# Optimization experiments

Measured on AMD Instinct MI355X. Metric: run time of the kernel, lower is better.

The kernel has to match this reference:

```python
import jax, jax.numpy as jnp
import numpy as np

EMBED_DIM = 768
NUM_HEADS = 12
HEAD_DIM = EMBED_DIM // NUM_HEADS
WINDOW = 64
B, S = 2, 2048


def setup_inputs() -> dict:
    key = jax.random.key(0)
    ks = jax.random.split(key, 8)
    xavier = 0.1 * np.sqrt(6.0 / (EMBED_DIM + EMBED_DIM))  # xavier_uniform with gain=0.1
    def lin_w(k):
        return jax.random.uniform(k, (EMBED_DIM, EMBED_DIM), jnp.float32, -xavier, xavier)
    return {
        "query": jax.random.normal(ks[0], (B, S, EMBED_DIM), jnp.float32),
        "key": jax.random.normal(ks[1], (B, S, EMBED_DIM), jnp.float32),
        "value": jax.random.normal(ks[2], (B, S, EMBED_DIM), jnp.float32),
        "key_padding_mask": jnp.zeros((B, S), dtype=bool),
        "Wq": lin_w(ks[3]), "bq": jnp.zeros((EMBED_DIM,), jnp.float32),
        "Wk": lin_w(ks[4]), "bk": jnp.zeros((EMBED_DIM,), jnp.float32),
        "Wv": lin_w(ks[5]), "bv": jnp.zeros((EMBED_DIM,), jnp.float32),
        "Wo": lin_w(ks[6]), "bo": jnp.zeros((EMBED_DIM,), jnp.float32),
    }


def reference(query, key, value, key_padding_mask, Wq, bq, Wk, bk, Wv, bv, Wo, bo):
    Bsz, Sl, E = query.shape
    H, D = NUM_HEADS, HEAD_DIM

    def proj(x, W, b):  # nn.Linear: x @ W.T + b, then split heads -> [B,H,S,D]
        return (x @ W.T + b).reshape(Bsz, Sl, H, D).transpose(0, 2, 1, 3)

    q = proj(query, Wq, bq)
    k = proj(key, Wk, bk)
    v = proj(value, Wv, bv)

    scale = float(D) ** -0.5
    scores = jnp.einsum("bhqd,bhkd->bhqk", q, k) * scale  # [B,H,S,S]

    idx = jnp.arange(Sl)
    win_mask = jnp.abs(idx[:, None] - idx[None, :]) > WINDOW  # True = masked out
    scores = jnp.where(win_mask[None, None], -10000.0, scores)
    scores = jnp.where(key_padding_mask[:, None, None, :], -10000.0, scores)
    scores = jnp.where(jnp.isnan(scores), -10000.0, scores)

    attn = jax.nn.softmax(scores, axis=-1) + 1e-6
    attn = jnp.where(jnp.isnan(attn), 1.0 / Sl, attn)

    ctx = jnp.einsum("bhqk,bhkd->bhqd", attn, v)
    ctx = ctx.transpose(0, 2, 1, 3).reshape(Bsz, Sl, E)
    out = ctx @ Wo.T + bo
    out = jnp.where(jnp.isnan(out), value, out)
    return out, attn
```

## Files before the change

### kernel.cpp

```cpp
#include <hip/hip_runtime.h>
#include <hip/hip_bf16.h>

#define EMBED 768
#define NHEADS 12
#define HDIM 64
#define WIN 64
#define BATCH 2
#define SEQ 2048
#define MROWS (BATCH*SEQ)
#define NBH (BATCH*NHEADS)
#define QT 32
#define KP 160
#define KPAD 168
#define SPAD 164

typedef __attribute__((ext_vector_type(8))) short short8;
typedef __attribute__((ext_vector_type(4))) float f32x4;

__device__ __forceinline__ float bf2f(unsigned short u) {
    union { unsigned int i; float f; } z;
    z.i = ((unsigned int)u) << 16;
    return z.f;
}
__device__ __forceinline__ unsigned short f2bf(float f) {
    __hip_bfloat16 h = __float2bfloat16(f);
    return *reinterpret_cast<unsigned short*>(&h);
}

__device__ __forceinline__ void gload16(const unsigned short* g, unsigned short* l) {
    __builtin_amdgcn_global_load_lds(
        (const __attribute__((address_space(1))) unsigned int*)g,
        (__attribute__((address_space(3))) unsigned int*)l,
        16, 0, 0);
}

struct CvtArgs {
    const float* src[4];
    unsigned short* dst[4];
};

__global__ __launch_bounds__(256) void cvt_w(CvtArgs ca) {
    const int n4 = EMBED * EMBED / 4;
    const int bper = (n4 + 255) / 256;
    int seg = blockIdx.x / bper;
    int i = (blockIdx.x - seg * bper) * 256 + threadIdx.x;
    if (i < n4) {
        float4 v = reinterpret_cast<const float4*>(ca.src[seg])[i];
        ushort4 o;
        o.x = f2bf(v.x); o.y = f2bf(v.y); o.z = f2bf(v.z); o.w = f2bf(v.w);
        reinterpret_cast<ushort4*>(ca.dst[seg])[i] = o;
    }
}

struct GArgs {
    const void* A[3];
    const unsigned short* Bm[3];
    const float* bias[3];
    void* C[3];
};

template<int F32OUT, int F32A>
__global__ __launch_bounds__(256) void gemm_nt(GArgs ga, int M, int N, int K) {
    const int z = blockIdx.z;
    const unsigned short* __restrict__ Bm = ga.Bm[z];
    const float* __restrict__ bias = ga.bias[z];

    const int bm = blockIdx.y * 128;
    const int bn = blockIdx.x * 128;

    __shared__ unsigned short As[128 * 32];
    __shared__ unsigned short Bs[128 * 32];

    const int tid = threadIdx.x;
    const int lane = tid & 63;
    const int wid = tid >> 6;
    const int wm = wid >> 1, wn = wid & 1;

    f32x4 acc[4][4] = {};

    const int fr = lane & 15;
    const int krow = (lane >> 4) * 8;

    for (int k0 = 0; k0 < K; k0 += 32) {
#pragma unroll
        for (int it = 0; it < 2; ++it) {
            int idx = it * 256 + tid;
            int r = idx >> 2;
            int c = (idx & 3) * 8;
            if (F32A) {
                const float* Af = (const float*)ga.A[z];
                const float4* src = reinterpret_cast<const float4*>(
                    Af + (size_t)(bm + r) * K + k0 + c);
                float4 v0 = src[0], v1 = src[1];
                short8 o;
                unsigned short* ou = reinterpret_cast<unsigned short*>(&o);
                ou[0] = f2bf(v0.x); ou[1] = f2bf(v0.y);
                ou[2] = f2bf(v0.z); ou[3] = f2bf(v0.w);
                ou[4] = f2bf(v1.x); ou[5] = f2bf(v1.y);
                ou[6] = f2bf(v1.z); ou[7] = f2bf(v1.w);
                *reinterpret_cast<short8*>(&As[idx * 8]) = o;
            } else {
                const unsigned short* Ab = (const unsigned short*)ga.A[z];
                gload16(Ab + (size_t)(bm + r) * K + k0 + c, &As[idx * 8]);
            }
            gload16(Bm + (size_t)(bn + r) * K + k0 + c, &Bs[idx * 8]);
        }
        __syncthreads();

        short8 af[4], bfv[4];
#pragma unroll
        for (int mf = 0; mf < 4; ++mf)
            af[mf] = *reinterpret_cast<const short8*>(&As[(wm * 64 + mf * 16 + fr) * 32 + krow]);
#pragma unroll
        for (int nf = 0; nf < 4; ++nf)
            bfv[nf] = *reinterpret_cast<const short8*>(&Bs[(wn * 64 + nf * 16 + fr) * 32 + krow]);
#pragma unroll
        for (int mf = 0; mf < 4; ++mf)
#pragma unroll
            for (int nf = 0; nf < 4; ++nf)
                acc[mf][nf] = __builtin_amdgcn_mfma_f32_16x16x32_bf16(
                    af[mf], bfv[nf], acc[mf][nf], 0, 0, 0);
        __syncthreads();
    }

    const int fq = lane >> 4;
#pragma unroll
    for (int mf = 0; mf < 4; ++mf)
#pragma unroll
        for (int nf = 0; nf < 4; ++nf) {
            int col = bn + wn * 64 + nf * 16 + fr;
            float bv = bias[col];
#pragma unroll
            for (int r = 0; r < 4; ++r) {
                int row = bm + wm * 64 + mf * 16 + fq * 4 + r;
                float v = acc[mf][nf][r] + bv;
                if (F32OUT)
                    reinterpret_cast<float*>(ga.C[z])[(size_t)row * N + col] = v;
                else
                    reinterpret_cast<unsigned short*>(ga.C[z])[(size_t)row * N + col] = f2bf(v);
            }
        }
}

__global__ __launch_bounds__(256) void sumv_kernel(const unsigned short* __restrict__ Vb,
                                                   float* __restrict__ sumV) {
    __shared__ float r[32][HDIM];
    const int bh = blockIdx.x;
    const int b = bh / NHEADS, h = bh % NHEADS;
    const int dg = (threadIdx.x & 7) * 8;
    const int r0 = threadIdx.x >> 3;
    float acc[8] = {};
    const unsigned short* vp = Vb + (size_t)(b * SEQ) * EMBED + h * HDIM + dg;
    for (int j = r0; j < SEQ; j += 32) {
        short8 v = *reinterpret_cast<const short8*>(vp + (size_t)j * EMBED);
#pragma unroll
        for (int e = 0; e < 8; ++e)
            acc[e] += bf2f(((const unsigned short*)&v)[e]);
    }
#pragma unroll
    for (int e = 0; e < 8; ++e) r[r0][dg + e] = acc[e];
    __syncthreads();
    if (threadIdx.x < HDIM) {
        float s = 0.f;
#pragma unroll
        for (int i = 0; i < 32; ++i) s += r[i][threadIdx.x];
        sumV[bh * HDIM + threadIdx.x] = s;
    }
}

__global__ __launch_bounds__(256, 3) void attn_mfma(
    const unsigned short* __restrict__ Q,
    const unsigned short* __restrict__ Kb,
    const unsigned short* __restrict__ Vb,
    const unsigned char* __restrict__ kpm,
    const float* __restrict__ sumV,
    float* __restrict__ attn_out,
    unsigned short* __restrict__ ctx) {
    const int qt = blockIdx.x;
    const int bh = blockIdx.y;
    const int h = bh % NHEADS;
    const int b = bh / NHEADS;
    const int q0 = qt * QT;
    const int kstart = max(q0 - WIN, 0);

    __shared__ float Sf[QT][SPAD];
    __shared__ unsigned short Pb[QT][KPAD];
    __shared__ unsigned short Vt[HDIM][KPAD];

    const int tid = threadIdx.x;
    const int l = tid & 63;
    const int w = tid >> 6;
    const int fr = l & 15;
    const int ksl = (l >> 4) * 8;

    const size_t base = (size_t)(b * SEQ) * EMBED + h * HDIM;

    {
        const int mf = w >> 1;
        const int nt0 = (w & 1) * 5;

        const unsigned short* qrow = Q + base + (size_t)(q0 + mf * 16 + fr) * EMBED;
        short8 aq0 = *reinterpret_cast<const short8*>(qrow + ksl);
        short8 aq1 = *reinterpret_cast<const short8*>(qrow + 32 + ksl);

        f32x4 sacc[5] = {};
#pragma unroll
        for (int t = 0; t < 5; ++t) {
            int jg = kstart + (nt0 + t) * 16 + fr;
            int jc = min(jg, SEQ - 1);
            const unsigned short* krow = Kb + base + (size_t)jc * EMBED;
            short8 b0 = *reinterpret_cast<const short8*>(krow + ksl);
            short8 b1 = *reinterpret_cast<const short8*>(krow + 32 + ksl);
            sacc[t] = __builtin_amdgcn_mfma_f32_16x16x32_bf16(aq0, b0, sacc[t], 0, 0, 0);
            sacc[t] = __builtin_amdgcn_mfma_f32_16x16x32_bf16(aq1, b1, sacc[t], 0, 0, 0);
        }

#pragma unroll
        for (int t = 0; t < 5; ++t) {
            int col = (nt0 + t) * 16 + fr;
            int jg = kstart + col;
            bool jvalid = (jg < SEQ);
            bool mk = jvalid && kpm[b * SEQ + jg];
#pragma unroll
            for (int r = 0; r < 4; ++r) {
                int rowl = mf * 16 + (l >> 4) * 4 + r;
                int qi = q0 + rowl;
                float s = sacc[t][r] * 0.125f;
                if (mk) s = -10000.f;
                int dd = qi - jg;
                if (!jvalid || dd > WIN || dd < -WIN) s = -1e30f;
                Sf[rowl][col] = s;
            }
        }

#pragma unroll
        for (int pass = 0; pass < 5; ++pass) {
            int jrel = pass * 32 + (tid >> 3);
            int jg = kstart + jrel;
            int dg = (tid & 7) * 8;
            short8 v = {};
            if (jg < SEQ)
                v = *reinterpret_cast<const short8*>(Vb + base + (size_t)jg * EMBED + dg);
#pragma unroll
            for (int e = 0; e < 8; ++e)
                Vt[dg + e][jrel] = ((const unsigned short*)&v)[e];
        }
    }
    __syncthreads();

    {
        const int row = tid >> 3;
        const int cg = tid & 7;
        float e[KP / 8];
        float m = -1e30f;
#pragma unroll
        for (int i = 0; i < KP / 8; ++i) {
            float s = Sf[row][cg + i * 8];
            e[i] = s;
            m = fmaxf(m, s);
        }
#pragma unroll
        for (int off = 1; off < 8; off <<= 1) m = fmaxf(m, __shfl_xor(m, off));
        float sum = 0.f;
#pragma unroll
        for (int i = 0; i < KP / 8; ++i) {
            e[i] = __expf(e[i] - m);
            sum += e[i];
        }
#pragma unroll
        for (int off = 1; off < 8; off <<= 1) sum += __shfl_xor(sum, off);
        float inv = 1.f / sum;
#pragma unroll
        for (int i = 0; i < KP / 8; ++i) {
            float p = e[i] * inv;
            int col = cg + i * 8;
            Sf[row][col] = p;
            Pb[row][col] = f2bf(p);
        }
    }
    __syncthreads();

    {
#pragma unroll
        for (int rr = 0; rr < QT / 4; ++rr) {
            int row = w * (QT / 4) + rr;
            int qi = q0 + row;
            int blo = max(qi - WIN, 0);
            int bhi = min(qi + WIN, SEQ - 1);
            float* __restrict__ orow = attn_out + ((size_t)bh * SEQ + qi) * SEQ;
#pragma unroll
            for (int seg = 0; seg < SEQ / 256; ++seg) {
                int c0 = seg * 256 + l * 4;
                f32x4 v = {1e-6f, 1e-6f, 1e-6f, 1e-6f};
                if (c0 + 3 >= blo && c0 <= bhi) {
#pragma unroll
                    for (int e = 0; e < 4; ++e) {
                        int c = c0 + e;
                        if (c >= blo && c <= bhi) v[e] = Sf[row][c - kstart] + 1e-6f;
                    }
                }
                __builtin_nontemporal_store(v, reinterpret_cast<f32x4*>(orow + c0));
            }
        }
    }

    {
        const int mf = w >> 1;
        const int nfb = (w & 1) * 2;
        f32x4 oacc[2] = {};
#pragma unroll
        for (int kk = 0; kk < KP / 32; ++kk) {
            short8 a = *reinterpret_cast<const short8*>(&Pb[mf * 16 + fr][kk * 32 + ksl]);
#pragma unroll
            for (int n2 = 0; n2 < 2; ++n2) {
                short8 bv = *reinterpret_cast<const short8*>(&Vt[(nfb + n2) * 16 + fr][kk * 32 + ksl]);
                oacc[n2] = __builtin_amdgcn_mfma_f32_16x16x32_bf16(a, bv, oacc[n2], 0, 0, 0);
            }
        }
#pragma unroll
        for (int n2 = 0; n2 < 2; ++n2) {
            int d = (nfb + n2) * 16 + fr;
            float sv = 1e-6f * sumV[bh * HDIM + d];
#pragma unroll
            for (int r = 0; r < 4; ++r) {
                int rowl = mf * 16 + (l >> 4) * 4 + r;
                ctx[base + (size_t)(q0 + rowl) * EMBED + d] = f2bf(oacc[n2][r] + sv);
            }
        }
    }
}

extern "C" void kernel_launch(void* const* d_in, const int* in_sizes, int n_in,
                              void* d_out, int out_size, void* d_ws, size_t ws_size,
                              hipStream_t stream) {
    const float* q_in = (const float*)d_in[0];
    const float* k_in = (const float*)d_in[1];
    const float* v_in = (const float*)d_in[2];
    const unsigned char* kpm = (const unsigned char*)d_in[3];
    const float* Wq = (const float*)d_in[4];
    const float* bq = (const float*)d_in[5];
    const float* Wk = (const float*)d_in[6];
    const float* bk = (const float*)d_in[7];
    const float* Wv = (const float*)d_in[8];
    const float* bv = (const float*)d_in[9];
    const float* Wo = (const float*)d_in[10];
    const float* bo = (const float*)d_in[11];

    char* ws = (char*)d_ws;
    size_t off = 0;
    auto alloc = [&](size_t bytes) {
        void* p = ws + off;
        off += (bytes + 255) & ~255ULL;
        return p;
    };
    const size_t XB = (size_t)MROWS * EMBED * 2;
    const size_t WB = (size_t)EMBED * EMBED * 2;
    unsigned short* wqb = (unsigned short*)alloc(WB);
    unsigned short* wkb = (unsigned short*)alloc(WB);
    unsigned short* wvb = (unsigned short*)alloc(WB);
    unsigned short* wob = (unsigned short*)alloc(WB);
    unsigned short* Qb = (unsigned short*)alloc(XB);
    unsigned short* Kb = (unsigned short*)alloc(XB);
    unsigned short* Vb = (unsigned short*)alloc(XB);
    unsigned short* ctx = (unsigned short*)alloc(XB);
    float* sumV = (float*)alloc((size_t)NBH * HDIM * 4);

    float* out0 = (float*)d_out;
    float* attn_out = out0 + (size_t)MROWS * EMBED;

    {
        CvtArgs ca;
        ca.src[0] = Wq; ca.src[1] = Wk; ca.src[2] = Wv; ca.src[3] = Wo;
        ca.dst[0] = wqb; ca.dst[1] = wkb; ca.dst[2] = wvb; ca.dst[3] = wob;
        int bper = (EMBED * EMBED / 4 + 255) / 256;
        cvt_w<<<dim3(4 * bper), dim3(256), 0, stream>>>(ca);
    }

    {
        GArgs ga;
        ga.A[0] = q_in; ga.A[1] = k_in; ga.A[2] = v_in;
        ga.Bm[0] = wqb; ga.Bm[1] = wkb; ga.Bm[2] = wvb;
        ga.bias[0] = bq; ga.bias[1] = bk; ga.bias[2] = bv;
        ga.C[0] = Qb; ga.C[1] = Kb; ga.C[2] = Vb;
        gemm_nt<0, 1><<<dim3(EMBED / 128, MROWS / 128, 3), dim3(256), 0, stream>>>(
            ga, MROWS, EMBED, EMBED);
    }

    sumv_kernel<<<dim3(NBH), dim3(256), 0, stream>>>(Vb, sumV);

    attn_mfma<<<dim3(SEQ / QT, NBH), dim3(256), 0, stream>>>(
        Qb, Kb, Vb, kpm, sumV, attn_out, ctx);

    {
        GArgs ga;
        ga.A[0] = ctx;  ga.A[1] = ctx;  ga.A[2] = ctx;
        ga.Bm[0] = wob; ga.Bm[1] = wob; ga.Bm[2] = wob;
        ga.bias[0] = bo; ga.bias[1] = bo; ga.bias[2] = bo;
        ga.C[0] = out0; ga.C[1] = out0; ga.C[2] = out0;
        gemm_nt<1, 0><<<dim3(EMBED / 128, MROWS / 128, 1), dim3(256), 0, stream>>>(
            ga, MROWS, EMBED, EMBED);
    }
}
```

Measured before the change: 183.0 us.

## Remap blocks across XCDs, async-load fp32 A tiles, hoist out-of-window attn fill

The GEMM now loads fp32 A tiles straight into LDS with global_load_lds, using an XOR swizzle, and converts them to bf16 when reading fragments, replacing the register-staged conversion. Both the GEMM and attention kernels remap flat block IDs so that contiguous panels or heads land on the same XCD, which is meant to improve L2 locality. The attention kernel writes the constant 1e-6 fill for out-of-window segments at kernel start, before compute, and the later pass only writes the segments inside the window. The remapping assumes grid sizes divisible by 8 and a fixed 192-blocks-per-XCD layout. The fp32 A tile doubles its LDS footprint.

```diff
diff --git a/kernel.cpp b/kernel.cpp
--- a/kernel.cpp
+++ b/kernel.cpp
@@ -27,7 +27,7 @@
     return *reinterpret_cast<unsigned short*>(&h);
 }
 
-__device__ __forceinline__ void gload16(const unsigned short* g, unsigned short* l) {
+__device__ __forceinline__ void gload16(const void* g, void* l) {
     __builtin_amdgcn_global_load_lds(
         (const __attribute__((address_space(1))) unsigned int*)g,
         (__attribute__((address_space(3))) unsigned int*)l,
@@ -61,14 +61,19 @@
 
 template<int F32OUT, int F32A>
 __global__ __launch_bounds__(256) void gemm_nt(GArgs ga, int M, int N, int K) {
-    const int z = blockIdx.z;
+    const int NPANEL = gridDim.y * gridDim.z;
+    const int flat = (blockIdx.z * gridDim.y + blockIdx.y) * gridDim.x + blockIdx.x;
+    const int xcd = flat & 7;
+    const int j = flat >> 3;
+    const int panel = xcd * (NPANEL >> 3) + j / gridDim.x;
+    const int z = panel / gridDim.y;
+    const int bm = (panel % gridDim.y) * 128;
+    const int bn = (j % gridDim.x) * 128;
+
     const unsigned short* __restrict__ Bm = ga.Bm[z];
     const float* __restrict__ bias = ga.bias[z];
 
-    const int bm = blockIdx.y * 128;
-    const int bn = blockIdx.x * 128;
-
-    __shared__ unsigned short As[128 * 32];
+    __shared__ alignas(16) unsigned char AsRaw[F32A ? 128 * 32 * 4 : 128 * 32 * 2];
     __shared__ unsigned short Bs[128 * 32];
 
     const int tid = threadIdx.x;
@@ -82,35 +87,57 @@
     const int krow = (lane >> 4) * 8;
 
     for (int k0 = 0; k0 < K; k0 += 32) {
+        if (F32A) {
+            const float* Af = (const float*)ga.A[z];
+            float* AsF = (float*)AsRaw;
+#pragma unroll
+            for (int it = 0; it < 4; ++it) {
+                int idx = it * 256 + tid;
+                int r = idx >> 3;
+                int cc = idx & 7;
+                int gcc = cc ^ (r & 7);
+                gload16(Af + (size_t)(bm + r) * K + k0 + gcc * 4, &AsF[idx * 4]);
+            }
+        } else {
+            const unsigned short* Ab = (const unsigned short*)ga.A[z];
+#pragma unroll
+            for (int it = 0; it < 2; ++it) {
+                int idx = it * 256 + tid;
+                int r = idx >> 2;
+                int c = (idx & 3) * 8;
+                gload16(Ab + (size_t)(bm + r) * K + k0 + c,
+                        (unsigned short*)AsRaw + idx * 8);
+            }
+        }
 #pragma unroll
         for (int it = 0; it < 2; ++it) {
             int idx = it * 256 + tid;
             int r = idx >> 2;
             int c = (idx & 3) * 8;
+            gload16(Bm + (size_t)(bn + r) * K + k0 + c, &Bs[idx * 8]);
+        }
+        __syncthreads();
+
+        short8 af[4], bfv[4];
+#pragma unroll
+        for (int mf = 0; mf < 4; ++mf) {
+            int r = wm * 64 + mf * 16 + fr;
             if (F32A) {
-                const float* Af = (const float*)ga.A[z];
-                const float4* src = reinterpret_cast<const float4*>(
-                    Af + (size_t)(bm + r) * K + k0 + c);
-                float4 v0 = src[0], v1 = src[1];
-                short8 o;
-                unsigned short* ou = reinterpret_cast<unsigned short*>(&o);
-                ou[0] = f2bf(v0.x); ou[1] = f2bf(v0.y);
-                ou[2] = f2bf(v0.z); ou[3] = f2bf(v0.w);
-                ou[4] = f2bf(v1.x); ou[5] = f2bf(v1.y);
-                ou[6] = f2bf(v1.z); ou[7] = f2bf(v1.w);
-                *reinterpret_cast<short8*>(&As[idx * 8]) = o;
+                const float* AsF = (const float*)AsRaw;
+                int kc0 = (lane >> 4) * 2;
+                int s0 = kc0 ^ (r & 7);
+                f32x4 v0 = *reinterpret_cast<const f32x4*>(&AsF[(r * 8 + s0) * 4]);
+                f32x4 v1 = *reinterpret_cast<const f32x4*>(&AsF[(r * 8 + (s0 ^ 1)) * 4]);
+                unsigned short* ou = reinterpret_cast<unsigned short*>(&af[mf]);
+                ou[0] = f2bf(v0[0]); ou[1] = f2bf(v0[1]);
+                ou[2] = f2bf(v0[2]); ou[3] = f2bf(v0[3]);
+                ou[4] = f2bf(v1[0]); ou[5] = f2bf(v1[1]);
+                ou[6] = f2bf(v1[2]); ou[7] = f2bf(v1[3]);
             } else {
-                const unsigned short* Ab = (const unsigned short*)ga.A[z];
-                gload16(Ab + (size_t)(bm + r) * K + k0 + c, &As[idx * 8]);
-            }
-            gload16(Bm + (size_t)(bn + r) * K + k0 + c, &Bs[idx * 8]);
-        }
-        __syncthreads();
-
-        short8 af[4], bfv[4];
-#pragma unroll
-        for (int mf = 0; mf < 4; ++mf)
-            af[mf] = *reinterpret_cast<const short8*>(&As[(wm * 64 + mf * 16 + fr) * 32 + krow]);
+                af[mf] = *reinterpret_cast<const short8*>(
+                    (const unsigned short*)AsRaw + r * 32 + krow);
+            }
+        }
 #pragma unroll
         for (int nf = 0; nf < 4; ++nf)
             bfv[nf] = *reinterpret_cast<const short8*>(&Bs[(wn * 64 + nf * 16 + fr) * 32 + krow]);
@@ -176,8 +203,10 @@
     const float* __restrict__ sumV,
     float* __restrict__ attn_out,
     unsigned short* __restrict__ ctx) {
-    const int qt = blockIdx.x;
-    const int bh = blockIdx.y;
+    const int flat = blockIdx.y * gridDim.x + blockIdx.x;
+    const int g2 = (flat & 7) * 192 + (flat >> 3);
+    const int bh = g2 >> 6;
+    const int qt = g2 & 63;
     const int h = bh % NHEADS;
     const int b = bh / NHEADS;
     const int q0 = qt * QT;
@@ -194,6 +223,24 @@
     const int ksl = (l >> 4) * 8;
 
     const size_t base = (size_t)(b * SEQ) * EMBED + h * HDIM;
+
+    {
+        const f32x4 fill = {1e-6f, 1e-6f, 1e-6f, 1e-6f};
+#pragma unroll
+        for (int rr = 0; rr < QT / 4; ++rr) {
+            int row = w * (QT / 4) + rr;
+            int qi = q0 + row;
+            int blo = max(qi - WIN, 0);
+            int bhi = min(qi + WIN, SEQ - 1);
+            float* __restrict__ orow = attn_out + ((size_t)bh * SEQ + qi) * SEQ;
+#pragma unroll
+            for (int seg = 0; seg < SEQ / 256; ++seg) {
+                if (seg * 256 + 255 >= blo && seg * 256 <= bhi) continue;
+                __builtin_nontemporal_store(
+                    fill, reinterpret_cast<f32x4*>(orow + seg * 256 + l * 4));
+            }
+        }
+    }
 
     {
         const int mf = w >> 1;
@@ -288,16 +335,15 @@
             int blo = max(qi - WIN, 0);
             int bhi = min(qi + WIN, SEQ - 1);
             float* __restrict__ orow = attn_out + ((size_t)bh * SEQ + qi) * SEQ;
-#pragma unroll
-            for (int seg = 0; seg < SEQ / 256; ++seg) {
+            int slo = blo >> 8;
+            int shi = bhi >> 8;
+            for (int seg = slo; seg <= shi; ++seg) {
                 int c0 = seg * 256 + l * 4;
                 f32x4 v = {1e-6f, 1e-6f, 1e-6f, 1e-6f};
-                if (c0 + 3 >= blo && c0 <= bhi) {
-#pragma unroll
-                    for (int e = 0; e < 4; ++e) {
-                        int c = c0 + e;
-                        if (c >= blo && c <= bhi) v[e] = Sf[row][c - kstart] + 1e-6f;
-                    }
+#pragma unroll
+                for (int e = 0; e < 4; ++e) {
+                    int c = c0 + e;
+                    if (c >= blo && c <= bhi) v[e] = Sf[row][c - kstart] + 1e-6f;
                 }
                 __builtin_nontemporal_store(v, reinterpret_cast<f32x4*>(orow + c0));
             }
```

Result: faster. 159.9 us (-12.6%).
